# Kernel tuning notes

Hardware: AMD Instinct MI355X
Metric: run time of the kernel (lower is better)

## Reference

```python
import jax, jax.numpy as jnp
import numpy as np

B, T, D, K = 8, 1024, 512, 1024
PRECISION = 0.1


def setup_inputs() -> dict:
    key = jax.random.key(0)
    kx, kc = jax.random.split(key)
    x = jax.random.normal(kx, (B, T, D), dtype=jnp.float32)
    codebook = jax.random.normal(kc, (K, D), dtype=jnp.float32)
    precision = PRECISION * jnp.ones((1,), dtype=jnp.float32)
    return {"x": x, "codebook": codebook, "precision": precision}


def reference(x, codebook, precision):
    # score[b,t,k] = -sum_d (x[b,t,d] - codebook[k,d])^2
    x_sq = jnp.sum(x * x, axis=-1, keepdims=True)            # [B,T,1]
    c_sq = jnp.sum(codebook * codebook, axis=-1)              # [K]
    xc = jnp.einsum('btd,kd->btk', x, codebook)               # [B,T,K] GEMM
    score = -(x_sq - 2.0 * xc + c_sq)                         # [B,T,K]
    return precision * score
```

## Files before the change

kernel.cpp:

```cpp
#include <hip/hip_runtime.h>

typedef unsigned short u16;
typedef __attribute__((ext_vector_type(8))) short short8;
typedef __attribute__((ext_vector_type(4))) float f32x4;

typedef void gvoid_t __attribute__((address_space(1)));
typedef void lvoid_t __attribute__((address_space(3)));

#define M_DIM 8192
#define N_DIM 1024
#define K_DIM 512

__device__ __forceinline__ void async_copy16(const void* g, void* l) {
  __builtin_amdgcn_global_load_lds((gvoid_t*)g, (lvoid_t*)l, 16, 0, 0);
}

__device__ __forceinline__ unsigned bf16bits(float v) {
  union { float f; unsigned u; } c; c.f = v;
  return (c.u + 0x7FFFu + ((c.u >> 16) & 1u)) >> 16;
}

__global__ __launch_bounds__(256) void cvt_sq_kernel(
    const float* __restrict__ x, const float* __restrict__ cb,
    u16* __restrict__ xb, u16* __restrict__ cbb,
    float* __restrict__ xsq, float* __restrict__ csq) {
  int row = blockIdx.x * 4 + (threadIdx.x >> 6);
  int lane = threadIdx.x & 63;
  const float* src; u16* dst; float* sq;
  if (row < M_DIM) {
    src = x + (size_t)row * K_DIM; dst = xb + (size_t)row * K_DIM; sq = xsq + row;
  } else {
    int r = row - M_DIM;
    src = cb + (size_t)r * K_DIM; dst = cbb + (size_t)r * K_DIM; sq = csq + r;
  }
  const float4* s4 = (const float4*)src;
  float4 v0 = s4[lane * 2];
  float4 v1 = s4[lane * 2 + 1];
  float f[8] = {v0.x, v0.y, v0.z, v0.w, v1.x, v1.y, v1.z, v1.w};
  float s = 0.f;
  unsigned pk[4];
#pragma unroll
  for (int i = 0; i < 4; i++) {
    s += f[2 * i] * f[2 * i] + f[2 * i + 1] * f[2 * i + 1];
    pk[i] = bf16bits(f[2 * i]) | (bf16bits(f[2 * i + 1]) << 16);
  }
  ((uint4*)dst)[lane] = make_uint4(pk[0], pk[1], pk[2], pk[3]);
#pragma unroll
  for (int off = 32; off > 0; off >>= 1) s += __shfl_xor(s, off, 64);
  if (lane == 0) *sq = s;
}

__global__ __launch_bounds__(256) void qgemm_kernel(
    const u16* __restrict__ A, const u16* __restrict__ B,
    const float* __restrict__ xsq, const float* __restrict__ csq,
    const float* __restrict__ prec, float* __restrict__ out) {
  __shared__ char lds[32768];
  const int tid = threadIdx.x;
  const int wave = tid >> 6, lane = tid & 63;
  const int m0 = blockIdx.y * 128, n0 = blockIdx.x * 128;
  const int wm = wave >> 1, wn = wave & 1;
  const int srow = lane >> 3;
  const int scol = ((lane & 7) ^ srow) * 8;
  const int ml = lane & 15, q = lane >> 4;

  f32x4 acc[4][4] = {};

  for (int k0 = 0; k0 < K_DIM; k0 += 64) {
#pragma unroll
    for (int c = wave; c < 16; c += 4) {
      const u16* ga = A + (size_t)(m0 + c * 8 + srow) * K_DIM + (k0 + scol);
      async_copy16(ga, lds + c * 1024);
      const u16* gb = B + (size_t)(n0 + c * 8 + srow) * K_DIM + (k0 + scol);
      async_copy16(gb, lds + 16384 + c * 1024);
    }
    __syncthreads();
#pragma unroll
    for (int kk = 0; kk < 2; kk++) {
      const int p = ((((kk << 2) | q) ^ (lane & 7)) << 4);
      short8 a[4], b[4];
#pragma unroll
      for (int i = 0; i < 4; i++) {
        a[i] = *(const short8*)(lds + (wm * 64 + i * 16 + ml) * 128 + p);
        b[i] = *(const short8*)(lds + 16384 + (wn * 64 + i * 16 + ml) * 128 + p);
      }
#pragma unroll
      for (int i = 0; i < 4; i++)
#pragma unroll
        for (int j = 0; j < 4; j++)
          acc[i][j] = __builtin_amdgcn_mfma_f32_16x16x32_bf16(a[i], b[j], acc[i][j], 0, 0, 0);
    }
    __syncthreads();
  }

  const float p = prec[0];
  float csv[4];
#pragma unroll
  for (int j = 0; j < 4; j++) csv[j] = csq[n0 + wn * 64 + j * 16 + ml];
#pragma unroll
  for (int i = 0; i < 4; i++) {
#pragma unroll
    for (int r = 0; r < 4; r++) {
      int row = m0 + wm * 64 + i * 16 + q * 4 + r;
      float xs = xsq[row];
      float* orow = out + (size_t)row * N_DIM + n0 + wn * 64 + ml;
#pragma unroll
      for (int j = 0; j < 4; j++)
        orow[j * 16] = p * (2.0f * acc[i][j][r] - xs - csv[j]);
    }
  }
}

extern "C" void kernel_launch(void* const* d_in, const int* in_sizes, int n_in,
                              void* d_out, int out_size, void* d_ws, size_t ws_size,
                              hipStream_t stream) {
  const float* x    = (const float*)d_in[0];
  const float* cb   = (const float*)d_in[1];
  const float* prec = (const float*)d_in[2];
  float* out = (float*)d_out;

  char* ws = (char*)d_ws;
  u16*   xb  = (u16*)(ws);
  u16*   cbb = (u16*)(ws + 8388608);
  float* xsq = (float*)(ws + 9437184);
  float* csq = (float*)(ws + 9469952);

  cvt_sq_kernel<<<2304, 256, 0, stream>>>(x, cb, xb, cbb, xsq, csq);
  qgemm_kernel<<<dim3(8, 64), 256, 0, stream>>>(xb, cbb, xsq, csq, prec, out);
}
```

Before: 91.13 us.

## Double-buffer LDS tiles in GEMM, use nontemporal output stores, coalesce conversion loads

The GEMM main loop now uses two 32KB LDS buffers. The async global-to-LDS copy for the next K tile is issued before computing on the current one, so global loads overlap MFMA work. The output epilogue uses nontemporal stores for the large fp32 result, and the csq/precision loads move before the loop. The conversion kernel switches to lane-strided float4 loads and uint2 stores for better coalescing. Doubling LDS per block to 64KB limits how many blocks can reside on each CU.

```diff
diff --git a/kernel.cpp b/kernel.cpp
--- a/kernel.cpp
+++ b/kernel.cpp
@@ -34,17 +34,15 @@
     src = cb + (size_t)r * K_DIM; dst = cbb + (size_t)r * K_DIM; sq = csq + r;
   }
   const float4* s4 = (const float4*)src;
-  float4 v0 = s4[lane * 2];
-  float4 v1 = s4[lane * 2 + 1];
-  float f[8] = {v0.x, v0.y, v0.z, v0.w, v1.x, v1.y, v1.z, v1.w};
-  float s = 0.f;
-  unsigned pk[4];
-#pragma unroll
-  for (int i = 0; i < 4; i++) {
-    s += f[2 * i] * f[2 * i] + f[2 * i + 1] * f[2 * i + 1];
-    pk[i] = bf16bits(f[2 * i]) | (bf16bits(f[2 * i + 1]) << 16);
-  }
-  ((uint4*)dst)[lane] = make_uint4(pk[0], pk[1], pk[2], pk[3]);
+  float4 v0 = s4[lane];
+  float4 v1 = s4[lane + 64];
+  float s = v0.x * v0.x + v0.y * v0.y + v0.z * v0.z + v0.w * v0.w +
+            v1.x * v1.x + v1.y * v1.y + v1.z * v1.z + v1.w * v1.w;
+  uint2* d2 = (uint2*)dst;
+  d2[lane]      = make_uint2(bf16bits(v0.x) | (bf16bits(v0.y) << 16),
+                             bf16bits(v0.z) | (bf16bits(v0.w) << 16));
+  d2[lane + 64] = make_uint2(bf16bits(v1.x) | (bf16bits(v1.y) << 16),
+                             bf16bits(v1.z) | (bf16bits(v1.w) << 16));
 #pragma unroll
   for (int off = 32; off > 0; off >>= 1) s += __shfl_xor(s, off, 64);
   if (lane == 0) *sq = s;
@@ -54,7 +52,7 @@
     const u16* __restrict__ A, const u16* __restrict__ B,
     const float* __restrict__ xsq, const float* __restrict__ csq,
     const float* __restrict__ prec, float* __restrict__ out) {
-  __shared__ char lds[32768];
+  __shared__ char lds[65536];
   const int tid = threadIdx.x;
   const int wave = tid >> 6, lane = tid & 63;
   const int m0 = blockIdx.y * 128, n0 = blockIdx.x * 128;
@@ -63,25 +61,38 @@
   const int scol = ((lane & 7) ^ srow) * 8;
   const int ml = lane & 15, q = lane >> 4;
 
-  f32x4 acc[4][4] = {};
-
-  for (int k0 = 0; k0 < K_DIM; k0 += 64) {
+  auto stage = [&](int k0, int buf) {
+    char* base = lds + buf * 32768;
 #pragma unroll
     for (int c = wave; c < 16; c += 4) {
       const u16* ga = A + (size_t)(m0 + c * 8 + srow) * K_DIM + (k0 + scol);
-      async_copy16(ga, lds + c * 1024);
+      async_copy16(ga, base + c * 1024);
       const u16* gb = B + (size_t)(n0 + c * 8 + srow) * K_DIM + (k0 + scol);
-      async_copy16(gb, lds + 16384 + c * 1024);
+      async_copy16(gb, base + 16384 + c * 1024);
     }
-    __syncthreads();
+  };
+
+  stage(0, 0);
+
+  const float p = prec[0];
+  float csv[4];
+#pragma unroll
+  for (int j = 0; j < 4; j++) csv[j] = csq[n0 + wn * 64 + j * 16 + ml];
+
+  f32x4 acc[4][4] = {};
+  __syncthreads();
+
+  for (int step = 0; step < 8; step++) {
+    if (step < 7) stage((step + 1) * 64, (step + 1) & 1);
+    const char* base = lds + (step & 1) * 32768;
 #pragma unroll
     for (int kk = 0; kk < 2; kk++) {
-      const int p = ((((kk << 2) | q) ^ (lane & 7)) << 4);
+      const int pcol = ((((kk << 2) | q) ^ (lane & 7)) << 4);
       short8 a[4], b[4];
 #pragma unroll
       for (int i = 0; i < 4; i++) {
-        a[i] = *(const short8*)(lds + (wm * 64 + i * 16 + ml) * 128 + p);
-        b[i] = *(const short8*)(lds + 16384 + (wn * 64 + i * 16 + ml) * 128 + p);
+        a[i] = *(const short8*)(base + (wm * 64 + i * 16 + ml) * 128 + pcol);
+        b[i] = *(const short8*)(base + 16384 + (wn * 64 + i * 16 + ml) * 128 + pcol);
       }
 #pragma unroll
       for (int i = 0; i < 4; i++)
@@ -92,10 +103,6 @@
     __syncthreads();
   }
 
-  const float p = prec[0];
-  float csv[4];
-#pragma unroll
-  for (int j = 0; j < 4; j++) csv[j] = csq[n0 + wn * 64 + j * 16 + ml];
 #pragma unroll
   for (int i = 0; i < 4; i++) {
 #pragma unroll
@@ -105,7 +112,8 @@
       float* orow = out + (size_t)row * N_DIM + n0 + wn * 64 + ml;
 #pragma unroll
       for (int j = 0; j < 4; j++)
-        orow[j * 16] = p * (2.0f * acc[i][j][r] - xs - csv[j]);
+        __builtin_nontemporal_store(p * (2.0f * acc[i][j][r] - xs - csv[j]),
+                                    orow + j * 16);
     }
   }
 }
```

Result: no change. 91.73 us (+0.7%).
